# Kernel optimization log

Hardware: AMD Instinct MI355X
Metric: run time of the kernel (lower is better)

## Reference

```python
import jax, jax.numpy as jnp
import numpy as np

D_THRESH = 0.5  # forward default d=0.5


def setup_inputs() -> dict:
    key = jax.random.key(0)
    C, P, D = 10, 1000, 1024
    # scale so pairwise distances (~sqrt(2D)*scale) straddle the 0.5 threshold
    feats = jax.random.normal(key, (C * P, D), dtype=jnp.float32) * 0.011
    ids_per_cls = jnp.arange(C * P, dtype=jnp.int64).reshape(C, P)
    return {"feats": feats, "ids_per_cls": ids_per_cls, "budget": 2000}


def reference(feats, ids_per_cls, budget):
    C, P = ids_per_cls.shape
    per_cls_budget = budget // C  # budget = int(budget / len(ids_per_cls_train))
    X = feats[ids_per_cls.reshape(-1)]  # [C*P, D] class-blocked representatives
    # pairwise euclidean distances (torch.cdist p=2), computed via gram trick
    sq = jnp.sum(X * X, axis=-1)  # [C*P]
    d2 = sq[:, None] + sq[None, :] - 2.0 * (X @ X.T)  # [C*P, C*P]
    dist = jnp.sqrt(jnp.maximum(d2, 0.0))
    # only count neighbors from OTHER classes (the per-class loop pops class i)
    cls = jnp.repeat(jnp.arange(C), P)  # [C*P]
    other = cls[:, None] != cls[None, :]  # [C*P, C*P] bool
    counts = jnp.sum((dist < D_THRESH) & other, axis=-1)  # [C*P] int
    counts = counts.reshape(C, P)
    # ascending sort by count, keep the `per_cls_budget` most-separated nodes
    order = jnp.argsort(counts, axis=-1)  # [C, P]
    sel = order[:, :per_cls_budget]  # [C, budget//C]
    ids_selected = jnp.take_along_axis(ids_per_cls, sel, axis=1).reshape(-1)
    return ids_selected, counts
```

## Files before the change

### kernel.cpp

```cpp
#include <hip/hip_runtime.h>

#define N_TOT 10000
#define CLS_P 1000
#define NC 10
#define D 1024

#define TM 128
#define DELTA 1.35e-5f
#define INV_SCALE2 4.8828125e-4f
#define ESC_CAP (1 << 22)
#define ESC_LOC 256
#define KCHUNKS (D / 32)
#define NTILE ((N_TOT + TM - 1) / TM)

typedef _Float16 f16x8 __attribute__((ext_vector_type(8)));
typedef float f32x4 __attribute__((ext_vector_type(4)));
typedef const __attribute__((address_space(1))) unsigned int* gptr_t;
typedef __attribute__((address_space(3))) unsigned int* lptr_t;

__global__ void zero_kernel(int* __restrict__ out, int n, int* __restrict__ esc_cnt) {
    int i = blockIdx.x * blockDim.x + threadIdx.x;
    if (i < n) out[i] = 0;
    if (i == 0) *esc_cnt = 0;
}

__global__ void prep_kernel(const float* __restrict__ feats, const int* __restrict__ ids,
                            unsigned short* __restrict__ Xh,
                            double* __restrict__ sqd, float* __restrict__ sqf) {
    int row = blockIdx.x;
    int id = ids[row];
    const float4* rp = (const float4*)(feats + (size_t)id * D);
    float4 v = rp[threadIdx.x];
    float f[4] = {v.x, v.y, v.z, v.w};
    ushort4 hv;
    unsigned short* hp = &hv.x;
    double s = 0.0;
    #pragma unroll
    for (int e = 0; e < 4; e++) {
        s += (double)f[e] * f[e];
        union { _Float16 h; unsigned short u; } cv;
        cv.h = (_Float16)(f[e] * 64.0f);
        hp[e] = cv.u;
    }
    *(ushort4*)(Xh + (size_t)row * D + threadIdx.x * 4) = hv;

    #pragma unroll
    for (int off = 32; off > 0; off >>= 1)
        s += __shfl_down(s, off, 64);
    __shared__ double wsum[4];
    int lane = threadIdx.x & 63, wv = threadIdx.x >> 6;
    if (lane == 0) wsum[wv] = s;
    __syncthreads();
    if (threadIdx.x == 0) {
        double t = wsum[0] + wsum[1] + wsum[2] + wsum[3];
        sqd[row] = t;
        sqf[row] = (float)t;
    }
}

__launch_bounds__(256, 3)
__global__ void count_kernel(const unsigned short* __restrict__ Xh,
                             const float* __restrict__ sqf,
                             int* __restrict__ counts,
                             int* __restrict__ esc_cnt, int2* __restrict__ esc_list) {
    int bid = blockIdx.y * gridDim.x + blockIdx.x;
    int it_t = 0, jt_t = 0;
    {
        int rem = bid, band = 0;
        while (true) {
            int h = NTILE - band * 8; if (h > 8) h = 8;
            int area = h * NTILE;
            if (rem < area) { it_t = band * 8 + rem % h; jt_t = rem / h; break; }
            rem -= area; band++;
        }
    }
    const int ib = it_t * TM, jb = jt_t * TM;
    if (jb < ib) return;

    {
        int ci0 = ib / CLS_P, ci1 = (ib + TM - 1) / CLS_P;
        int cj0 = jb / CLS_P, cj1 = (jb + TM - 1) / CLS_P;
        if (ci0 == ci1 && cj0 == cj1 && ci0 == cj0) return;
    }

    __shared__ unsigned short S[3 * 8192];
    __shared__ int cred_i[TM], cred_j[TM];
    __shared__ int esc_n, esc_base;
    __shared__ int2 esc_buf[ESC_LOC];

    const int tid = threadIdx.x;
    const int lane = tid & 63, w = tid >> 6;
    const int wi = (w & 1) * 64, wj = (w >> 1) * 64;
    const int quad = lane >> 4, col = lane & 15;

    if (tid == 0) esc_n = 0;

    const int warr = w >> 1;
    const int w01 = w & 1;
    const int rl0 = lane >> 2;
    const int slot = lane & 3;
    const int q = (slot - rl0 - (rl0 >> 2)) & 3;
    const int rowbase = warr ? jb : ib;

    const unsigned short* src[4];
    #pragma unroll
    for (int b = 0; b < 4; b++) {
        int grow = rowbase + b * 32 + w01 * 16 + rl0;
        if (grow > N_TOT - 1) grow = N_TOT - 1;
        src[b] = Xh + (size_t)grow * D + q * 8;
    }

#define STAGE(KC_, BUFBASE_)                                                     \
    {                                                                            \
        _Pragma("unroll")                                                        \
        for (int b = 0; b < 4; b++) {                                            \
            __builtin_amdgcn_global_load_lds(                                    \
                (gptr_t)(src[b] + (KC_) * 32),                                   \
                (lptr_t)((BUFBASE_) + warr * 4096 + b * 1024 + w01 * 512),       \
                16, 0, 0);                                                       \
        }                                                                        \
    }

#define FRAGS_(AH, BH, BUFBASE_)                                                 \
    {                                                                            \
        _Pragma("unroll")                                                        \
        for (int t = 0; t < 4; t++) {                                            \
            int rA = wi + t * 16 + col;                                          \
            int sA = (quad + rA + (rA >> 2)) & 3;                                \
            AH[t] = *(const f16x8*)((BUFBASE_) + rA * 32 + sA * 8);              \
            int rB = wj + t * 16 + col;                                          \
            int sB = (quad + rB + (rB >> 2)) & 3;                                \
            BH[t] = *(const f16x8*)((BUFBASE_) + 4096 + rB * 32 + sB * 8);       \
        }                                                                        \
    }

#define MFMA16_(AH, BH)                                                          \
    {                                                                            \
        _Pragma("unroll")                                                        \
        for (int it = 0; it < 4; it++)                                           \
            _Pragma("unroll")                                                    \
            for (int jt = 0; jt < 4; jt++)                                       \
                acc[it][jt] = __builtin_amdgcn_mfma_f32_16x16x32_f16(AH[it], BH[jt], acc[it][jt], 0, 0, 0); \
    }

#define WAIT4_BAR asm volatile("s_waitcnt vmcnt(4)\ns_barrier" ::: "memory")
#define WAIT0_BAR asm volatile("s_waitcnt vmcnt(0)\ns_barrier" ::: "memory")

    f32x4 acc[4][4];
    #pragma unroll
    for (int it = 0; it < 4; it++)
        #pragma unroll
        for (int jt = 0; jt < 4; jt++)
            acc[it][jt] = (f32x4){0.f, 0.f, 0.f, 0.f};

    f16x8 ah0[4], bh0[4], ah1[4], bh1[4];

    unsigned short* p0 = S;
    unsigned short* p1 = S + 8192;
    unsigned short* p2 = S + 16384;

    STAGE(0, p0);
    STAGE(1, p1);
    WAIT4_BAR;
    FRAGS_(ah0, bh0, p0);

    for (int kc = 0; kc < KCHUNKS - 2; kc += 2) {
        STAGE(kc + 2, p2);
        WAIT4_BAR;
        FRAGS_(ah1, bh1, p1);
        MFMA16_(ah0, bh0);
        { unsigned short* t = p0; p0 = p1; p1 = p2; p2 = t; }

        STAGE(kc + 3, p2);
        WAIT4_BAR;
        FRAGS_(ah0, bh0, p1);
        MFMA16_(ah1, bh1);
        { unsigned short* t = p0; p0 = p1; p1 = p2; p2 = t; }
    }
    WAIT0_BAR;
    FRAGS_(ah1, bh1, p1);
    MFMA16_(ah0, bh0);
    MFMA16_(ah1, bh1);

    if (tid < TM) { cred_i[tid] = 0; cred_j[tid] = 0; }
    __syncthreads();

    const float thr_lo = 0.25f - DELTA;
    const float thr_hi = 0.25f + DELTA;
    const bool diag = (ib == jb);

    float sqj[4];
    int clsj[4], jv[4], jidx[4];
    #pragma unroll
    for (int jt = 0; jt < 4; jt++) {
        int j = jb + wj + jt * 16 + col;
        jidx[jt] = j;
        jv[jt] = (j < N_TOT);
        sqj[jt] = jv[jt] ? sqf[j] : 0.f;
        clsj[jt] = j / CLS_P;
    }

    int cj[4] = {0, 0, 0, 0};

    #pragma unroll
    for (int it = 0; it < 4; it++) {
        #pragma unroll
        for (int r = 0; r < 4; r++) {
            int irow = wi + it * 16 + quad * 4 + r;
            int i = ib + irow;
            bool iv = (i < N_TOT);
            float sqi = iv ? sqf[i] : 0.f;
            int clsi = i / CLS_P;
            int ci = 0;
            #pragma unroll
            for (int jt = 0; jt < 4; jt++) {
                int j = jidx[jt];
                bool ok = iv && jv[jt] && (clsj[jt] != clsi) && (!diag || j > i);
                float d2 = sqi + sqj[jt] - acc[it][jt][r] * INV_SCALE2;
                bool in = ok && (d2 < thr_lo);
                bool esc = ok && !in && (d2 < thr_hi);
                ci += in ? 1 : 0;
                cj[jt] += in ? 1 : 0;
                if (esc) {
                    int k = atomicAdd(&esc_n, 1);
                    if (k < ESC_LOC) {
                        esc_buf[k] = make_int2(i, j);
                    } else {
                        int idx = atomicAdd(esc_cnt, 1);
                        if (idx < ESC_CAP) esc_list[idx] = make_int2(i, j);
                    }
                }
            }
            ci += __shfl_xor(ci, 1, 64);
            ci += __shfl_xor(ci, 2, 64);
            ci += __shfl_xor(ci, 4, 64);
            ci += __shfl_xor(ci, 8, 64);
            if (col == 0 && ci) atomicAdd(&cred_i[irow], ci);
        }
    }
    #pragma unroll
    for (int jt = 0; jt < 4; jt++) {
        int v = cj[jt];
        v += __shfl_xor(v, 16, 64);
        v += __shfl_xor(v, 32, 64);
        if (quad == 0 && v) atomicAdd(&cred_j[wj + jt * 16 + col], v);
    }
    __syncthreads();
    if (tid < TM) {
        int i = ib + tid;
        if (i < N_TOT && cred_i[tid]) atomicAdd(&counts[i], cred_i[tid]);
        int j = jb + tid;
        if (j < N_TOT && cred_j[tid]) atomicAdd(&counts[j], cred_j[tid]);
    }
    if (tid == 0) {
        int n = esc_n; if (n > ESC_LOC) n = ESC_LOC;
        esc_n = n;
        esc_base = atomicAdd(esc_cnt, n);
    }
    __syncthreads();
    for (int k = tid; k < esc_n; k += 256) {
        int idx = esc_base + k;
        if (idx < ESC_CAP) esc_list[idx] = esc_buf[k];
    }
}

__global__ void escalate_kernel(const float* __restrict__ feats, const int* __restrict__ ids,
                                const double* __restrict__ sqd,
                                const int* __restrict__ esc_cnt, const int2* __restrict__ esc_list,
                                int* __restrict__ counts) {
    int n = *esc_cnt;
    if (n > ESC_CAP) n = ESC_CAP;
    int lane = threadIdx.x & 63;
    int sub = lane >> 4;
    int l16 = lane & 15;
    int wglob = (blockIdx.x * blockDim.x + threadIdx.x) >> 6;
    int W = (gridDim.x * blockDim.x) >> 6;
    for (int p0 = wglob * 4; p0 < n; p0 += W * 4) {
        int p = p0 + sub;
        bool act = (p < n);
        int2 pr = act ? esc_list[p] : make_int2(0, 0);
        const float* xi = feats + (size_t)ids[pr.x] * D;
        const float* xj = feats + (size_t)ids[pr.y] * D;
        double s = 0.0;
        int k0 = l16 * 64;
        #pragma unroll
        for (int k = 0; k < 64; k += 4) {
            float4 a = *(const float4*)(xi + k0 + k);
            float4 b = *(const float4*)(xj + k0 + k);
            s += (double)a.x * b.x + (double)a.y * b.y + (double)a.z * b.z + (double)a.w * b.w;
        }
        s += __shfl_xor(s, 1, 64);
        s += __shfl_xor(s, 2, 64);
        s += __shfl_xor(s, 4, 64);
        s += __shfl_xor(s, 8, 64);
        if (act && l16 == 0) {
            double d2 = sqd[pr.x] + sqd[pr.y] - 2.0 * s;
            if (d2 < 0.25) {
                atomicAdd(&counts[pr.x], 1);
                atomicAdd(&counts[pr.y], 1);
            }
        }
    }
}

__global__ void sel_kernel(const int* __restrict__ counts, const int* __restrict__ ids,
                           int* __restrict__ out_ids, int pcb) {
    int c = blockIdx.x;
    __shared__ int lc[CLS_P];
    for (int p = threadIdx.x; p < CLS_P; p += blockDim.x)
        lc[p] = counts[c * CLS_P + p];
    __syncthreads();
    int p = threadIdx.x;
    if (p < CLS_P) {
        int cp = lc[p];
        int rank = 0;
        for (int qq = 0; qq < CLS_P; qq++) {
            int cq = lc[qq];
            rank += (cq < cp) || (cq == cp && qq < p);
        }
        if (rank < pcb)
            out_ids[c * pcb + rank] = ids[c * CLS_P + p];
    }
}

extern "C" void kernel_launch(void* const* d_in, const int* in_sizes, int n_in,
                              void* d_out, int out_size, void* d_ws, size_t ws_size,
                              hipStream_t stream) {
    const float* feats = (const float*)d_in[0];
    const int* ids = (const int*)d_in[1];
    int budget = out_size - N_TOT;
    int pcb = budget / NC;
    int* out = (int*)d_out;
    int* counts_out = out + NC * pcb;

    char* ws = (char*)d_ws;
    const size_t XH_OFF = 0;
    const size_t SQD_OFF = XH_OFF + (size_t)N_TOT * D * 2;
    const size_t SQF_OFF = SQD_OFF + (size_t)N_TOT * 8;
    const size_t ESCC_OFF = (SQF_OFF + (size_t)N_TOT * 4 + 63) & ~(size_t)63;
    const size_t ESCL_OFF = ESCC_OFF + 64;

    unsigned short* Xh = (unsigned short*)(ws + XH_OFF);
    double* sqd = (double*)(ws + SQD_OFF);
    float* sqf = (float*)(ws + SQF_OFF);
    int* esc_cnt = (int*)(ws + ESCC_OFF);
    int2* esc_list = (int2*)(ws + ESCL_OFF);

    zero_kernel<<<(out_size + 255) / 256, 256, 0, stream>>>(out, out_size, esc_cnt);
    prep_kernel<<<N_TOT, 256, 0, stream>>>(feats, ids, Xh, sqd, sqf);
    dim3 grid(NTILE, NTILE);
    count_kernel<<<grid, 256, 0, stream>>>(Xh, sqf, counts_out, esc_cnt, esc_list);
    escalate_kernel<<<4096, 256, 0, stream>>>(feats, ids, sqd, esc_cnt, esc_list, counts_out);
    sel_kernel<<<NC, 1024, 0, stream>>>(counts_out, ids, out, pcb);
}
```

Measured before the change: 342.3 us.

## Fuse escalation recheck into count kernel, drop global escalation list

Pairs whose fp16 distance falls near the threshold are now rechecked in double precision inside the count kernel, at the end of each tile, from the shared-memory buffer. This removes the separate escalate kernel launch, the global escalation counter and list, and their global writes and reads. Pairs beyond the 256 local slots are handled inline by a serial per-thread 1024-element double dot product, which could be very slow if any tile overflows. The tile tail now also does feats reads and double-precision work, lengthening each block.

```diff
diff --git a/kernel.cpp b/kernel.cpp
--- a/kernel.cpp
+++ b/kernel.cpp
@@ -8,7 +8,6 @@
 #define TM 128
 #define DELTA 1.35e-5f
 #define INV_SCALE2 4.8828125e-4f
-#define ESC_CAP (1 << 22)
 #define ESC_LOC 256
 #define KCHUNKS (D / 32)
 #define NTILE ((N_TOT + TM - 1) / TM)
@@ -18,10 +17,9 @@
 typedef const __attribute__((address_space(1))) unsigned int* gptr_t;
 typedef __attribute__((address_space(3))) unsigned int* lptr_t;
 
-__global__ void zero_kernel(int* __restrict__ out, int n, int* __restrict__ esc_cnt) {
+__global__ void zero_kernel(int* __restrict__ out, int n) {
     int i = blockIdx.x * blockDim.x + threadIdx.x;
     if (i < n) out[i] = 0;
-    if (i == 0) *esc_cnt = 0;
 }
 
 __global__ void prep_kernel(const float* __restrict__ feats, const int* __restrict__ ids,
@@ -61,8 +59,10 @@
 __launch_bounds__(256, 3)
 __global__ void count_kernel(const unsigned short* __restrict__ Xh,
                              const float* __restrict__ sqf,
-                             int* __restrict__ counts,
-                             int* __restrict__ esc_cnt, int2* __restrict__ esc_list) {
+                             const double* __restrict__ sqd,
+                             const float* __restrict__ feats,
+                             const int* __restrict__ ids,
+                             int* __restrict__ counts) {
     int bid = blockIdx.y * gridDim.x + blockIdx.x;
     int it_t = 0, jt_t = 0;
     {
@@ -85,7 +85,7 @@
 
     __shared__ unsigned short S[3 * 8192];
     __shared__ int cred_i[TM], cred_j[TM];
-    __shared__ int esc_n, esc_base;
+    __shared__ int esc_n;
     __shared__ int2 esc_buf[ESC_LOC];
 
     const int tid = threadIdx.x;
@@ -226,8 +226,14 @@
                     if (k < ESC_LOC) {
                         esc_buf[k] = make_int2(i, j);
                     } else {
-                        int idx = atomicAdd(esc_cnt, 1);
-                        if (idx < ESC_CAP) esc_list[idx] = make_int2(i, j);
+                        const float* xi = feats + (size_t)ids[i] * D;
+                        const float* xj = feats + (size_t)ids[j] * D;
+                        double s = 0.0;
+                        for (int kk = 0; kk < D; kk++) s += (double)xi[kk] * xj[kk];
+                        if (sqd[i] + sqd[j] - 2.0 * s < 0.25) {
+                            atomicAdd(&counts[i], 1);
+                            atomicAdd(&counts[j], 1);
+                        }
                     }
                 }
             }
@@ -252,33 +258,12 @@
         int j = jb + tid;
         if (j < N_TOT && cred_j[tid]) atomicAdd(&counts[j], cred_j[tid]);
     }
-    if (tid == 0) {
-        int n = esc_n; if (n > ESC_LOC) n = ESC_LOC;
-        esc_n = n;
-        esc_base = atomicAdd(esc_cnt, n);
-    }
-    __syncthreads();
-    for (int k = tid; k < esc_n; k += 256) {
-        int idx = esc_base + k;
-        if (idx < ESC_CAP) esc_list[idx] = esc_buf[k];
-    }
-}
-
-__global__ void escalate_kernel(const float* __restrict__ feats, const int* __restrict__ ids,
-                                const double* __restrict__ sqd,
-                                const int* __restrict__ esc_cnt, const int2* __restrict__ esc_list,
-                                int* __restrict__ counts) {
-    int n = *esc_cnt;
-    if (n > ESC_CAP) n = ESC_CAP;
-    int lane = threadIdx.x & 63;
-    int sub = lane >> 4;
-    int l16 = lane & 15;
-    int wglob = (blockIdx.x * blockDim.x + threadIdx.x) >> 6;
-    int W = (gridDim.x * blockDim.x) >> 6;
-    for (int p0 = wglob * 4; p0 < n; p0 += W * 4) {
-        int p = p0 + sub;
-        bool act = (p < n);
-        int2 pr = act ? esc_list[p] : make_int2(0, 0);
+    __syncthreads();
+
+    int n = esc_n; if (n > ESC_LOC) n = ESC_LOC;
+    const int sub = lane >> 4, l16 = lane & 15;
+    for (int p = w * 4 + sub; p < n; p += 16) {
+        int2 pr = esc_buf[p];
         const float* xi = feats + (size_t)ids[pr.x] * D;
         const float* xj = feats + (size_t)ids[pr.y] * D;
         double s = 0.0;
@@ -293,7 +278,7 @@
         s += __shfl_xor(s, 2, 64);
         s += __shfl_xor(s, 4, 64);
         s += __shfl_xor(s, 8, 64);
-        if (act && l16 == 0) {
+        if (l16 == 0) {
             double d2 = sqd[pr.x] + sqd[pr.y] - 2.0 * s;
             if (d2 < 0.25) {
                 atomicAdd(&counts[pr.x], 1);
@@ -337,19 +322,14 @@
     const size_t XH_OFF = 0;
     const size_t SQD_OFF = XH_OFF + (size_t)N_TOT * D * 2;
     const size_t SQF_OFF = SQD_OFF + (size_t)N_TOT * 8;
-    const size_t ESCC_OFF = (SQF_OFF + (size_t)N_TOT * 4 + 63) & ~(size_t)63;
-    const size_t ESCL_OFF = ESCC_OFF + 64;
 
     unsigned short* Xh = (unsigned short*)(ws + XH_OFF);
     double* sqd = (double*)(ws + SQD_OFF);
     float* sqf = (float*)(ws + SQF_OFF);
-    int* esc_cnt = (int*)(ws + ESCC_OFF);
-    int2* esc_list = (int2*)(ws + ESCL_OFF);
-
-    zero_kernel<<<(out_size + 255) / 256, 256, 0, stream>>>(out, out_size, esc_cnt);
+
+    zero_kernel<<<(out_size + 255) / 256, 256, 0, stream>>>(out, out_size);
     prep_kernel<<<N_TOT, 256, 0, stream>>>(feats, ids, Xh, sqd, sqf);
     dim3 grid(NTILE, NTILE);
-    count_kernel<<<grid, 256, 0, stream>>>(Xh, sqf, counts_out, esc_cnt, esc_list);
-    escalate_kernel<<<4096, 256, 0, stream>>>(feats, ids, sqd, esc_cnt, esc_list, counts_out);
+    count_kernel<<<grid, 256, 0, stream>>>(Xh, sqf, sqd, feats, ids, counts_out);
     sel_kernel<<<NC, 1024, 0, stream>>>(counts_out, ids, out, pcb);
 }
```

Result: no change. 341.4 us (-0.3%).
